# Kernel tuning notes

Hardware: AMD Instinct MI355X
Metric: run time of the kernel (lower is better)

## Reference

```python
import jax, jax.numpy as jnp
import numpy as np
from jax import lax

N_GAUSS = 32768
M_POINTS = 8192
BLOCK = 256
MAX_SCALE = 0.02
BG = -1.0


def setup_inputs() -> dict:
    key = jax.random.key(0)
    k = jax.random.split(key, 6)
    # query points in [-1, 1]^3 (forward maps them to [0,1]^3)
    x = jax.random.uniform(k[0], (M_POINTS, 3), jnp.float32) * 2.0 - 1.0
    xyz = jax.random.uniform(k[1], (N_GAUSS, 3), jnp.float32)          # means in [0,1]^3
    weight_raw = jax.random.normal(k[2], (N_GAUSS, 1), jnp.float32)
    scaling_raw = jax.random.normal(k[3], (N_GAUSS, 3), jnp.float32) * 0.3 + jnp.log(0.01)
    rotation_raw = jax.random.normal(k[4], (N_GAUSS, 4), jnp.float32)
    values_raw = jax.random.normal(k[5], (N_GAUSS, 1), jnp.float32)
    return {"x": x, "xyz": xyz, "weight_raw": weight_raw,
            "scaling_raw": scaling_raw, "rotation_raw": rotation_raw,
            "values_raw": values_raw}


def _quat_to_rotmat(q):
    # q: [N,4] normalized quaternion (w, x, y, z)
    w, x, y, z = q[:, 0], q[:, 1], q[:, 2], q[:, 3]
    r00 = 1 - 2 * (y * y + z * z); r01 = 2 * (x * y - w * z); r02 = 2 * (x * z + w * y)
    r10 = 2 * (x * y + w * z); r11 = 1 - 2 * (x * x + z * z); r12 = 2 * (y * z - w * x)
    r20 = 2 * (x * z - w * y); r21 = 2 * (y * z + w * x); r22 = 1 - 2 * (x * x + y * y)
    return jnp.stack([jnp.stack([r00, r01, r02], -1),
                      jnp.stack([r10, r11, r12], -1),
                      jnp.stack([r20, r21, r22], -1)], -2)  # [N,3,3]


def _splat(x, xyz, weight_raw, scaling_raw, rotation_raw, values_raw):
    p = (x + 1.0) / 2.0  # [M,3] in [0,1]^3
    # activations (match VEGS properties)
    s = jnp.exp(scaling_raw)                                  # [N,3]
    r = jnp.linalg.norm(s, axis=1, keepdims=True) + 1e-8
    r_soft = MAX_SCALE * jnp.tanh(r / MAX_SCALE)
    s = s * (r_soft / r)                                      # capped scales
    q = rotation_raw / (jnp.linalg.norm(rotation_raw, axis=1, keepdims=True) + 1e-12)
    R = _quat_to_rotmat(q)                                    # [N,3,3]
    inv_cov = jnp.einsum('nij,nj,nkj->nik', R, 1.0 / (s * s), R)  # Sigma^-1 = R S^-2 R^T
    w = jax.nn.sigmoid(weight_raw)[:, 0]                      # [N]
    v = jax.nn.sigmoid(values_raw)[:, 0]                      # [N]

    def block_fn(_, pb):
        # pb: [B,3]
        d = pb[:, None, :] - xyz[None, :, :]                  # [B,N,3]
        quad = jnp.einsum('bni,nij,bnj->bn', d, inv_cov, d)   # Mahalanobis^2
        alpha = w[None, :] * jnp.exp(-0.5 * quad)             # [B,N]
        num = alpha @ v                                       # [B]
        den = jnp.sum(alpha, axis=1)                          # [B]
        yb = jnp.where(den > 1e-8, num, BG)                   # empty cells -> bg = -1
        return None, yb

    nb = M_POINTS // BLOCK
    _, ys = lax.scan(block_fn, None, p.reshape(nb, BLOCK, 3))
    return ys.reshape(-1, 1)


def reference(x, xyz, weight_raw, scaling_raw, rotation_raw, values_raw):
    return _splat(x, xyz, weight_raw, scaling_raw, rotation_raw, values_raw)
```

## Files before the change

### kernel.cpp

```cpp
#include <hip/hip_runtime.h>

#define NG 32768
#define MP 8192
#define BG_VAL (-1.0f)
#define MAX_SCALE 0.02f

#define HALF_LOG2E 0.72134752044448170f
#define LOG2E      1.44269504088896340f

#define NC 4
#define NCELL (NC * NC * NC)
#define CELLW 0.25f
#define INV_CELLW 4.0f
#define RADF 7.899f

#define NSG 16
#define SCG 512
#define GCAP (NSG * SCG)
#define NSP 4
#define SCP 96
#define PCAP (NSP * SCP)

__device__ __forceinline__ float fast_rcp(float x)  { return __builtin_amdgcn_rcpf(x); }
__device__ __forceinline__ float fast_exp2(float x) { return __builtin_amdgcn_exp2f(x); }
__device__ __forceinline__ float fast_exp(float x)  { return fast_exp2(x * LOG2E); }
__device__ __forceinline__ float fast_sigmoid(float x) { return fast_rcp(1.0f + fast_exp(-x)); }

__global__ __launch_bounds__(256) void vegs_build(
    const float* __restrict__ x,
    const float* __restrict__ xyz,
    const float* __restrict__ weight_raw,
    const float* __restrict__ scaling_raw,
    const float* __restrict__ rotation_raw,
    const float* __restrict__ values_raw,
    float4* __restrict__ gp,
    float4* __restrict__ gr,
    float4* __restrict__ px4)
{
    const int tid = blockIdx.x * 256 + threadIdx.x;

    if (tid < NG) {
        const int n = tid;
        float s0 = fast_exp(scaling_raw[n * 3 + 0]);
        float s1 = fast_exp(scaling_raw[n * 3 + 1]);
        float s2 = fast_exp(scaling_raw[n * 3 + 2]);
        float r = sqrtf(s0 * s0 + s1 * s1 + s2 * s2) + 1e-8f;
        float y = r * (1.0f / MAX_SCALE);
        float E = fast_exp2(2.0f * LOG2E * y);
        float th = (E - 1.0f) * fast_rcp(E + 1.0f);
        float k = (MAX_SCALE * th) * fast_rcp(r);
        s0 *= k; s1 *= k; s2 *= k;

        float i0 = fast_rcp(s0 * s0);
        float i1 = fast_rcp(s1 * s1);
        float i2 = fast_rcp(s2 * s2);

        float qw = rotation_raw[n * 4 + 0];
        float qx = rotation_raw[n * 4 + 1];
        float qy = rotation_raw[n * 4 + 2];
        float qz = rotation_raw[n * 4 + 3];
        float qn = sqrtf(qw * qw + qx * qx + qy * qy + qz * qz) + 1e-12f;
        float iq = fast_rcp(qn);
        qw *= iq; qx *= iq; qy *= iq; qz *= iq;

        float r00 = 1.0f - 2.0f * (qy * qy + qz * qz);
        float r01 = 2.0f * (qx * qy - qw * qz);
        float r02 = 2.0f * (qx * qz + qw * qy);
        float r10 = 2.0f * (qx * qy + qw * qz);
        float r11 = 1.0f - 2.0f * (qx * qx + qz * qz);
        float r12 = 2.0f * (qy * qz - qw * qx);
        float r20 = 2.0f * (qx * qz - qw * qy);
        float r21 = 2.0f * (qy * qz + qw * qx);
        float r22 = 1.0f - 2.0f * (qx * qx + qy * qy);

        float G00 = r00 * r00 * i0 + r01 * r01 * i1 + r02 * r02 * i2;
        float G11 = r10 * r10 * i0 + r11 * r11 * i1 + r12 * r12 * i2;
        float G22 = r20 * r20 * i0 + r21 * r21 * i1 + r22 * r22 * i2;
        float G01 = r00 * r10 * i0 + r01 * r11 * i1 + r02 * r12 * i2;
        float G02 = r00 * r20 * i0 + r01 * r21 * i1 + r02 * r22 * i2;
        float G12 = r10 * r20 * i0 + r11 * r21 * i1 + r12 * r22 * i2;

        float w  = fast_sigmoid(weight_raw[n]);
        float v  = fast_sigmoid(values_raw[n]);
        float m0 = xyz[n * 3 + 0];
        float m1 = xyz[n * 3 + 1];
        float m2 = xyz[n * 3 + 2];

        const float c = HALF_LOG2E;
        float h0 = 2.0f * c * (G00 * m0 + G01 * m1 + G02 * m2);
        float h1 = 2.0f * c * (G01 * m0 + G11 * m1 + G12 * m2);
        float h2 = 2.0f * c * (G02 * m0 + G12 * m1 + G22 * m2);
        float k0 = -0.5f * (h0 * m0 + h1 * m1 + h2 * m2);

        gp[n * 3 + 0] = make_float4(-c * G00, -c * G11, -c * G22, -2.0f * c * G01);
        gp[n * 3 + 1] = make_float4(-2.0f * c * G02, -2.0f * c * G12, h0, h1);
        gp[n * 3 + 2] = make_float4(h2, k0, w, w * v);

        float smax = fmaxf(s0, fmaxf(s1, s2));
        gr[n] = make_float4(m0, m1, m2, RADF * smax);
    } else if (tid < NG + MP) {
        const int m = tid - NG;
        float p0 = (x[m * 3 + 0] + 1.0f) * 0.5f;
        float p1 = (x[m * 3 + 1] + 1.0f) * 0.5f;
        float p2 = (x[m * 3 + 2] + 1.0f) * 0.5f;
        int cx = min(NC - 1, max(0, (int)(p0 * INV_CELLW)));
        int cy = min(NC - 1, max(0, (int)(p1 * INV_CELLW)));
        int cz = min(NC - 1, max(0, (int)(p2 * INV_CELLW)));
        int cell = cx + NC * (cy + NC * cz);
        px4[m] = make_float4(p0, p1, p2, __int_as_float(cell));
    }
}

__global__ __launch_bounds__(64) void vegs_bin(
    const float4* __restrict__ gr,
    const float4* __restrict__ px4,
    unsigned short* __restrict__ glist,
    float4* __restrict__ spt,
    int* __restrict__ gcount,
    int* __restrict__ pcount)
{
    const int bid  = blockIdx.x;
    const int lane = threadIdx.x;

    if (bid < NCELL * NSG) {
        const int c = bid / NSG;
        const int s = bid - c * NSG;
        const int cx = c & 3, cy = (c >> 2) & 3, cz = c >> 4;
        const float lo0 = cx * CELLW, hi0 = lo0 + CELLW;
        const float lo1 = cy * CELLW, hi1 = lo1 + CELLW;
        const float lo2 = cz * CELLW, hi2 = lo2 + CELLW;
        unsigned short* __restrict__ slab = glist + (size_t)c * GCAP + s * SCG;

        const int beg = s * (NG / NSG);
        const int end = beg + (NG / NSG);
        int cnt = 0;
        #pragma unroll 4
        for (int base = beg; base < end; base += 64) {
            float4 g = gr[base + lane];
            float dx = fmaxf(fmaxf(lo0 - g.x, g.x - hi0), 0.0f);
            float dy = fmaxf(fmaxf(lo1 - g.y, g.y - hi1), 0.0f);
            float dz = fmaxf(fmaxf(lo2 - g.z, g.z - hi2), 0.0f);
            bool hit = (dx * dx + dy * dy + dz * dz) <= g.w * g.w;
            unsigned long long mask = __ballot(hit);
            int pos = cnt + __popcll(mask & ((1ULL << lane) - 1ULL));
            if (hit && pos < SCG) slab[pos] = (unsigned short)(base + lane);
            cnt += __popcll(mask);
        }
        if (lane == 0) gcount[c * NSG + s] = min(cnt, SCG);
    } else {
        const int pb = bid - NCELL * NSG;
        const int c = pb / NSP;
        const int s = pb - c * NSP;
        float4* __restrict__ slab = spt + (size_t)c * PCAP + s * SCP;

        const int beg = s * (MP / NSP);
        const int end = beg + (MP / NSP);
        int cnt = 0;
        #pragma unroll 4
        for (int base = beg; base < end; base += 64) {
            float4 P = px4[base + lane];
            bool hit = (__float_as_int(P.w) == c);
            unsigned long long mask = __ballot(hit);
            int pos = cnt + __popcll(mask & ((1ULL << lane) - 1ULL));
            if (hit && pos < SCP)
                slab[pos] = make_float4(P.x, P.y, P.z, __int_as_float(base + lane));
            cnt += __popcll(mask);
        }
        if (lane == 0) pcount[c * NSP + s] = min(cnt, SCP);
    }
}

__global__ __launch_bounds__(64) void vegs_cellmain(
    const float4* __restrict__ gp,
    const float4* __restrict__ spt,
    const unsigned short* __restrict__ glist,
    const int* __restrict__ gcount,
    const int* __restrict__ pcount,
    float2* __restrict__ partial)
{
    const int c    = blockIdx.x;
    const int yw   = blockIdx.y;
    const int k    = blockIdx.z;
    const int lane = threadIdx.x;
    const int s    = yw >> 1;
    const int half = yw & 1;

    const int np = pcount[c * NSP + s];
    if (half * 64 >= np) return;

    const int  pi     = half * 64 + lane;
    const bool active = pi < np;
    const int  slot   = c * PCAP + s * SCP + (active ? pi : np - 1);

    float4 P = spt[slot];
    const float p0 = P.x, p1 = P.y, p2 = P.z;

    const unsigned short* __restrict__ slab = glist + (size_t)c * GCAP + k * SCG;
    const int glen = gcount[c * NSG + k];

    float num = 0.0f, den = 0.0f;

    #pragma unroll 4
    for (int j = 0; j < glen; ++j) {
        int gid = slab[j];
        float4 A0 = gp[gid * 3 + 0];
        float4 A1 = gp[gid * 3 + 1];
        float4 A2 = gp[gid * 3 + 2];

        float t0 = fmaf(A0.x, p0, A1.z);
        t0 = fmaf(A0.w, p1, t0);
        t0 = fmaf(A1.x, p2, t0);
        float t1 = fmaf(A0.y, p1, A1.w);
        t1 = fmaf(A1.y, p2, t1);
        float t2 = fmaf(A0.z, p2, A2.x);
        float q = fmaf(p0, t0, A2.y);
        q = fmaf(p1, t1, q);
        q = fmaf(p2, t2, q);

        float e = fast_exp2(q);
        den = fmaf(A2.z, e, den);
        num = fmaf(A2.w, e, num);
    }

    if (active)
        partial[(size_t)k * (NCELL * PCAP) + c * PCAP + s * SCP + pi] =
            make_float2(num, den);
}

__global__ __launch_bounds__(256) void vegs_reduce(
    const float2* __restrict__ partial,
    const float4* __restrict__ spt,
    const int* __restrict__ pcount,
    float* __restrict__ out)
{
    const int slot = blockIdx.x * 256 + threadIdx.x;
    const int c   = slot / PCAP;
    const int rem = slot - c * PCAP;
    const int s   = rem / SCP;
    const int pi  = rem - s * SCP;
    if (pi >= pcount[c * NSP + s]) return;

    float num = 0.0f, den = 0.0f;
    #pragma unroll
    for (int k = 0; k < NSG; ++k) {
        float2 p = partial[(size_t)k * (NCELL * PCAP) + slot];
        num += p.x;
        den += p.y;
    }
    int orig = __float_as_int(spt[slot].w);
    out[orig] = (den > 1e-8f) ? num : BG_VAL;
}

extern "C" void kernel_launch(void* const* d_in, const int* in_sizes, int n_in,
                              void* d_out, int out_size, void* d_ws, size_t ws_size,
                              hipStream_t stream) {
    const float* x            = (const float*)d_in[0];
    const float* xyz          = (const float*)d_in[1];
    const float* weight_raw   = (const float*)d_in[2];
    const float* scaling_raw  = (const float*)d_in[3];
    const float* rotation_raw = (const float*)d_in[4];
    const float* values_raw   = (const float*)d_in[5];
    float* out = (float*)d_out;

    char* ws = (char*)d_ws;
    size_t off = 0;
    float4* gp    = (float4*)(ws + off); off += (size_t)NG * 3 * sizeof(float4);
    float4* gr    = (float4*)(ws + off); off += (size_t)NG * sizeof(float4);
    float4* px4   = (float4*)(ws + off); off += (size_t)MP * sizeof(float4);
    float4* spt   = (float4*)(ws + off); off += (size_t)NCELL * PCAP * sizeof(float4);
    float2* partial = (float2*)(ws + off); off += (size_t)NSG * NCELL * PCAP * sizeof(float2);
    unsigned short* glist = (unsigned short*)(ws + off); off += (size_t)NCELL * GCAP * 2;
    int* gcount = (int*)(ws + off); off += NCELL * NSG * sizeof(int);
    int* pcount = (int*)(ws + off); off += NCELL * NSP * sizeof(int);

    vegs_build<<<(NG + MP) / 256, 256, 0, stream>>>(
        x, xyz, weight_raw, scaling_raw, rotation_raw, values_raw, gp, gr, px4);

    vegs_bin<<<NCELL * NSG + NCELL * NSP, 64, 0, stream>>>(
        gr, px4, glist, spt, gcount, pcount);

    dim3 mg(NCELL, NSP * 2, NSG);
    vegs_cellmain<<<mg, 64, 0, stream>>>(gp, spt, glist, gcount, pcount, partial);

    vegs_reduce<<<NCELL * PCAP / 256, 256, 0, stream>>>(partial, spt, pcount, out);
}
```

Measured before the change: 119.1 us.

## Compact per-cell gaussian parameter slabs and process two points per thread

The binning pass now copies each hit gaussian's 48-byte parameter record into a contiguous per-cell slab, replacing the index list. The main loop therefore streams the slab sequentially instead of doing indirect gathers. Each thread evaluates two query points per gaussian load, using a compacted per-cell point index built from prefix sums of the sub-slab counts. The gaussian split changes from 16 slabs of 512 to 32 slabs of 256, and point cell classification moves from the build kernel into the bin kernel. This trades more workspace and bin-time writes for fewer loads per evaluation in the hot loop, and doubles the partial buffer the reduction reads.

```diff
diff --git a/kernel.cpp b/kernel.cpp
--- a/kernel.cpp
+++ b/kernel.cpp
@@ -9,13 +9,13 @@
 #define LOG2E      1.44269504088896340f
 
 #define NC 4
-#define NCELL (NC * NC * NC)
+#define NCELL 64
 #define CELLW 0.25f
 #define INV_CELLW 4.0f
 #define RADF 7.899f
 
-#define NSG 16
-#define SCG 512
+#define NSG 32
+#define SCG 256
 #define GCAP (NSG * SCG)
 #define NSP 4
 #define SCP 96
@@ -27,94 +27,81 @@
 __device__ __forceinline__ float fast_sigmoid(float x) { return fast_rcp(1.0f + fast_exp(-x)); }
 
 __global__ __launch_bounds__(256) void vegs_build(
-    const float* __restrict__ x,
     const float* __restrict__ xyz,
     const float* __restrict__ weight_raw,
     const float* __restrict__ scaling_raw,
     const float* __restrict__ rotation_raw,
     const float* __restrict__ values_raw,
     float4* __restrict__ gp,
-    float4* __restrict__ gr,
-    float4* __restrict__ px4)
+    float4* __restrict__ gr)
 {
-    const int tid = blockIdx.x * 256 + threadIdx.x;
-
-    if (tid < NG) {
-        const int n = tid;
-        float s0 = fast_exp(scaling_raw[n * 3 + 0]);
-        float s1 = fast_exp(scaling_raw[n * 3 + 1]);
-        float s2 = fast_exp(scaling_raw[n * 3 + 2]);
-        float r = sqrtf(s0 * s0 + s1 * s1 + s2 * s2) + 1e-8f;
-        float y = r * (1.0f / MAX_SCALE);
-        float E = fast_exp2(2.0f * LOG2E * y);
-        float th = (E - 1.0f) * fast_rcp(E + 1.0f);
-        float k = (MAX_SCALE * th) * fast_rcp(r);
-        s0 *= k; s1 *= k; s2 *= k;
-
-        float i0 = fast_rcp(s0 * s0);
-        float i1 = fast_rcp(s1 * s1);
-        float i2 = fast_rcp(s2 * s2);
-
-        float qw = rotation_raw[n * 4 + 0];
-        float qx = rotation_raw[n * 4 + 1];
-        float qy = rotation_raw[n * 4 + 2];
-        float qz = rotation_raw[n * 4 + 3];
-        float qn = sqrtf(qw * qw + qx * qx + qy * qy + qz * qz) + 1e-12f;
-        float iq = fast_rcp(qn);
-        qw *= iq; qx *= iq; qy *= iq; qz *= iq;
-
-        float r00 = 1.0f - 2.0f * (qy * qy + qz * qz);
-        float r01 = 2.0f * (qx * qy - qw * qz);
-        float r02 = 2.0f * (qx * qz + qw * qy);
-        float r10 = 2.0f * (qx * qy + qw * qz);
-        float r11 = 1.0f - 2.0f * (qx * qx + qz * qz);
-        float r12 = 2.0f * (qy * qz - qw * qx);
-        float r20 = 2.0f * (qx * qz - qw * qy);
-        float r21 = 2.0f * (qy * qz + qw * qx);
-        float r22 = 1.0f - 2.0f * (qx * qx + qy * qy);
-
-        float G00 = r00 * r00 * i0 + r01 * r01 * i1 + r02 * r02 * i2;
-        float G11 = r10 * r10 * i0 + r11 * r11 * i1 + r12 * r12 * i2;
-        float G22 = r20 * r20 * i0 + r21 * r21 * i1 + r22 * r22 * i2;
-        float G01 = r00 * r10 * i0 + r01 * r11 * i1 + r02 * r12 * i2;
-        float G02 = r00 * r20 * i0 + r01 * r21 * i1 + r02 * r22 * i2;
-        float G12 = r10 * r20 * i0 + r11 * r21 * i1 + r12 * r22 * i2;
-
-        float w  = fast_sigmoid(weight_raw[n]);
-        float v  = fast_sigmoid(values_raw[n]);
-        float m0 = xyz[n * 3 + 0];
-        float m1 = xyz[n * 3 + 1];
-        float m2 = xyz[n * 3 + 2];
-
-        const float c = HALF_LOG2E;
-        float h0 = 2.0f * c * (G00 * m0 + G01 * m1 + G02 * m2);
-        float h1 = 2.0f * c * (G01 * m0 + G11 * m1 + G12 * m2);
-        float h2 = 2.0f * c * (G02 * m0 + G12 * m1 + G22 * m2);
-        float k0 = -0.5f * (h0 * m0 + h1 * m1 + h2 * m2);
-
-        gp[n * 3 + 0] = make_float4(-c * G00, -c * G11, -c * G22, -2.0f * c * G01);
-        gp[n * 3 + 1] = make_float4(-2.0f * c * G02, -2.0f * c * G12, h0, h1);
-        gp[n * 3 + 2] = make_float4(h2, k0, w, w * v);
-
-        float smax = fmaxf(s0, fmaxf(s1, s2));
-        gr[n] = make_float4(m0, m1, m2, RADF * smax);
-    } else if (tid < NG + MP) {
-        const int m = tid - NG;
-        float p0 = (x[m * 3 + 0] + 1.0f) * 0.5f;
-        float p1 = (x[m * 3 + 1] + 1.0f) * 0.5f;
-        float p2 = (x[m * 3 + 2] + 1.0f) * 0.5f;
-        int cx = min(NC - 1, max(0, (int)(p0 * INV_CELLW)));
-        int cy = min(NC - 1, max(0, (int)(p1 * INV_CELLW)));
-        int cz = min(NC - 1, max(0, (int)(p2 * INV_CELLW)));
-        int cell = cx + NC * (cy + NC * cz);
-        px4[m] = make_float4(p0, p1, p2, __int_as_float(cell));
-    }
+    const int n = blockIdx.x * 256 + threadIdx.x;
+    if (n >= NG) return;
+
+    float s0 = fast_exp(scaling_raw[n * 3 + 0]);
+    float s1 = fast_exp(scaling_raw[n * 3 + 1]);
+    float s2 = fast_exp(scaling_raw[n * 3 + 2]);
+    float r = sqrtf(s0 * s0 + s1 * s1 + s2 * s2) + 1e-8f;
+    float y = r * (1.0f / MAX_SCALE);
+    float E = fast_exp2(2.0f * LOG2E * y);
+    float th = (E - 1.0f) * fast_rcp(E + 1.0f);
+    float k = (MAX_SCALE * th) * fast_rcp(r);
+    s0 *= k; s1 *= k; s2 *= k;
+
+    float i0 = fast_rcp(s0 * s0);
+    float i1 = fast_rcp(s1 * s1);
+    float i2 = fast_rcp(s2 * s2);
+
+    float qw = rotation_raw[n * 4 + 0];
+    float qx = rotation_raw[n * 4 + 1];
+    float qy = rotation_raw[n * 4 + 2];
+    float qz = rotation_raw[n * 4 + 3];
+    float qn = sqrtf(qw * qw + qx * qx + qy * qy + qz * qz) + 1e-12f;
+    float iq = fast_rcp(qn);
+    qw *= iq; qx *= iq; qy *= iq; qz *= iq;
+
+    float r00 = 1.0f - 2.0f * (qy * qy + qz * qz);
+    float r01 = 2.0f * (qx * qy - qw * qz);
+    float r02 = 2.0f * (qx * qz + qw * qy);
+    float r10 = 2.0f * (qx * qy + qw * qz);
+    float r11 = 1.0f - 2.0f * (qx * qx + qz * qz);
+    float r12 = 2.0f * (qy * qz - qw * qx);
+    float r20 = 2.0f * (qx * qz - qw * qy);
+    float r21 = 2.0f * (qy * qz + qw * qx);
+    float r22 = 1.0f - 2.0f * (qx * qx + qy * qy);
+
+    float G00 = r00 * r00 * i0 + r01 * r01 * i1 + r02 * r02 * i2;
+    float G11 = r10 * r10 * i0 + r11 * r11 * i1 + r12 * r12 * i2;
+    float G22 = r20 * r20 * i0 + r21 * r21 * i1 + r22 * r22 * i2;
+    float G01 = r00 * r10 * i0 + r01 * r11 * i1 + r02 * r12 * i2;
+    float G02 = r00 * r20 * i0 + r01 * r21 * i1 + r02 * r22 * i2;
+    float G12 = r10 * r20 * i0 + r11 * r21 * i1 + r12 * r22 * i2;
+
+    float w  = fast_sigmoid(weight_raw[n]);
+    float v  = fast_sigmoid(values_raw[n]);
+    float m0 = xyz[n * 3 + 0];
+    float m1 = xyz[n * 3 + 1];
+    float m2 = xyz[n * 3 + 2];
+
+    const float c = HALF_LOG2E;
+    float h0 = 2.0f * c * (G00 * m0 + G01 * m1 + G02 * m2);
+    float h1 = 2.0f * c * (G01 * m0 + G11 * m1 + G12 * m2);
+    float h2 = 2.0f * c * (G02 * m0 + G12 * m1 + G22 * m2);
+    float k0 = -0.5f * (h0 * m0 + h1 * m1 + h2 * m2);
+
+    gp[n * 3 + 0] = make_float4(-c * G00, -c * G11, -c * G22, -2.0f * c * G01);
+    gp[n * 3 + 1] = make_float4(-2.0f * c * G02, -2.0f * c * G12, h0, h1);
+    gp[n * 3 + 2] = make_float4(h2, k0, w, w * v);
+
+    float smax = fmaxf(s0, fmaxf(s1, s2));
+    gr[n] = make_float4(m0, m1, m2, RADF * smax);
 }
 
 __global__ __launch_bounds__(64) void vegs_bin(
+    const float* __restrict__ x,
     const float4* __restrict__ gr,
-    const float4* __restrict__ px4,
-    unsigned short* __restrict__ glist,
+    const float4* __restrict__ gp,
+    float4* __restrict__ cslab,
     float4* __restrict__ spt,
     int* __restrict__ gcount,
     int* __restrict__ pcount)
@@ -129,24 +116,29 @@
         const float lo0 = cx * CELLW, hi0 = lo0 + CELLW;
         const float lo1 = cy * CELLW, hi1 = lo1 + CELLW;
         const float lo2 = cz * CELLW, hi2 = lo2 + CELLW;
-        unsigned short* __restrict__ slab = glist + (size_t)c * GCAP + s * SCG;
+        float4* __restrict__ slab = cslab + ((size_t)c * GCAP + s * SCG) * 3;
 
         const int beg = s * (NG / NSG);
         const int end = beg + (NG / NSG);
         int cnt = 0;
         #pragma unroll 4
         for (int base = beg; base < end; base += 64) {
-            float4 g = gr[base + lane];
+            const int gid = base + lane;
+            float4 g = gr[gid];
             float dx = fmaxf(fmaxf(lo0 - g.x, g.x - hi0), 0.0f);
             float dy = fmaxf(fmaxf(lo1 - g.y, g.y - hi1), 0.0f);
             float dz = fmaxf(fmaxf(lo2 - g.z, g.z - hi2), 0.0f);
             bool hit = (dx * dx + dy * dy + dz * dz) <= g.w * g.w;
             unsigned long long mask = __ballot(hit);
             int pos = cnt + __popcll(mask & ((1ULL << lane) - 1ULL));
-            if (hit && pos < SCG) slab[pos] = (unsigned short)(base + lane);
+            if (hit && pos < SCG) {
+                slab[pos * 3 + 0] = gp[gid * 3 + 0];
+                slab[pos * 3 + 1] = gp[gid * 3 + 1];
+                slab[pos * 3 + 2] = gp[gid * 3 + 2];
+            }
             cnt += __popcll(mask);
         }
-        if (lane == 0) gcount[c * NSG + s] = min(cnt, SCG);
+        if (lane == 0) gcount[bid] = min(cnt, SCG);
     } else {
         const int pb = bid - NCELL * NSG;
         const int c = pb / NSP;
@@ -158,73 +150,102 @@
         int cnt = 0;
         #pragma unroll 4
         for (int base = beg; base < end; base += 64) {
-            float4 P = px4[base + lane];
-            bool hit = (__float_as_int(P.w) == c);
+            const int m = base + lane;
+            float p0 = (x[m * 3 + 0] + 1.0f) * 0.5f;
+            float p1 = (x[m * 3 + 1] + 1.0f) * 0.5f;
+            float p2 = (x[m * 3 + 2] + 1.0f) * 0.5f;
+            int cx = min(NC - 1, max(0, (int)(p0 * INV_CELLW)));
+            int cy = min(NC - 1, max(0, (int)(p1 * INV_CELLW)));
+            int cz = min(NC - 1, max(0, (int)(p2 * INV_CELLW)));
+            bool hit = (cx + NC * (cy + NC * cz)) == c;
             unsigned long long mask = __ballot(hit);
             int pos = cnt + __popcll(mask & ((1ULL << lane) - 1ULL));
             if (hit && pos < SCP)
-                slab[pos] = make_float4(P.x, P.y, P.z, __int_as_float(base + lane));
+                slab[pos] = make_float4(p0, p1, p2, __int_as_float(m));
             cnt += __popcll(mask);
         }
-        if (lane == 0) pcount[c * NSP + s] = min(cnt, SCP);
+        if (lane == 0) pcount[pb] = min(cnt, SCP);
     }
 }
 
 __global__ __launch_bounds__(64) void vegs_cellmain(
-    const float4* __restrict__ gp,
+    const float4* __restrict__ cslab,
     const float4* __restrict__ spt,
-    const unsigned short* __restrict__ glist,
     const int* __restrict__ gcount,
     const int* __restrict__ pcount,
     float2* __restrict__ partial)
 {
     const int c    = blockIdx.x;
-    const int yw   = blockIdx.y;
+    const int pb   = blockIdx.y;
     const int k    = blockIdx.z;
     const int lane = threadIdx.x;
-    const int s    = yw >> 1;
-    const int half = yw & 1;
-
-    const int np = pcount[c * NSP + s];
-    if (half * 64 >= np) return;
-
-    const int  pi     = half * 64 + lane;
-    const bool active = pi < np;
-    const int  slot   = c * PCAP + s * SCP + (active ? pi : np - 1);
-
-    float4 P = spt[slot];
-    const float p0 = P.x, p1 = P.y, p2 = P.z;
-
-    const unsigned short* __restrict__ slab = glist + (size_t)c * GCAP + k * SCG;
+
+    const int n0 = pcount[c * NSP + 0];
+    const int n1 = pcount[c * NSP + 1];
+    const int n2 = pcount[c * NSP + 2];
+    const int n3 = pcount[c * NSP + 3];
+    const int c1 = n0, c2 = c1 + n1, c3 = c2 + n2;
+    const int nt = c3 + n3;
+    if (pb * 128 >= nt) return;
+
+    const int  piA  = pb * 128 + lane;
+    const int  piB  = piA + 64;
+    const bool actA = piA < nt;
+    const bool actB = piB < nt;
+    const int  peA  = actA ? piA : 0;
+    const int  peB  = actB ? piB : 0;
+
+    int sA = (peA >= c1) + (peA >= c2) + (peA >= c3);
+    int cumA = (sA == 0) ? 0 : ((sA == 1) ? c1 : ((sA == 2) ? c2 : c3));
+    int sB = (peB >= c1) + (peB >= c2) + (peB >= c3);
+    int cumB = (sB == 0) ? 0 : ((sB == 1) ? c1 : ((sB == 2) ? c2 : c3));
+
+    float4 PA = spt[c * PCAP + sA * SCP + (peA - cumA)];
+    float4 PB = spt[c * PCAP + sB * SCP + (peB - cumB)];
+    const float a0 = PA.x, a1 = PA.y, a2 = PA.z;
+    const float b0 = PB.x, b1 = PB.y, b2 = PB.z;
+
+    const float4* __restrict__ base = cslab + ((size_t)c * GCAP + k * SCG) * 3;
     const int glen = gcount[c * NSG + k];
 
-    float num = 0.0f, den = 0.0f;
+    float numA = 0.0f, denA = 0.0f;
+    float numB = 0.0f, denB = 0.0f;
 
     #pragma unroll 4
     for (int j = 0; j < glen; ++j) {
-        int gid = slab[j];
-        float4 A0 = gp[gid * 3 + 0];
-        float4 A1 = gp[gid * 3 + 1];
-        float4 A2 = gp[gid * 3 + 2];
-
-        float t0 = fmaf(A0.x, p0, A1.z);
-        t0 = fmaf(A0.w, p1, t0);
-        t0 = fmaf(A1.x, p2, t0);
-        float t1 = fmaf(A0.y, p1, A1.w);
-        t1 = fmaf(A1.y, p2, t1);
-        float t2 = fmaf(A0.z, p2, A2.x);
-        float q = fmaf(p0, t0, A2.y);
-        q = fmaf(p1, t1, q);
-        q = fmaf(p2, t2, q);
-
-        float e = fast_exp2(q);
-        den = fmaf(A2.z, e, den);
-        num = fmaf(A2.w, e, num);
+        float4 A0 = base[j * 3 + 0];
+        float4 A1 = base[j * 3 + 1];
+        float4 A2 = base[j * 3 + 2];
+
+        float t0 = fmaf(A0.x, a0, A1.z);
+        t0 = fmaf(A0.w, a1, t0);
+        t0 = fmaf(A1.x, a2, t0);
+        float t1 = fmaf(A0.y, a1, A1.w);
+        t1 = fmaf(A1.y, a2, t1);
+        float t2 = fmaf(A0.z, a2, A2.x);
+        float qA = fmaf(a0, t0, A2.y);
+        qA = fmaf(a1, t1, qA);
+        qA = fmaf(a2, t2, qA);
+        float eA = fast_exp2(qA);
+        denA = fmaf(A2.z, eA, denA);
+        numA = fmaf(A2.w, eA, numA);
+
+        float u0 = fmaf(A0.x, b0, A1.z);
+        u0 = fmaf(A0.w, b1, u0);
+        u0 = fmaf(A1.x, b2, u0);
+        float u1 = fmaf(A0.y, b1, A1.w);
+        u1 = fmaf(A1.y, b2, u1);
+        float u2 = fmaf(A0.z, b2, A2.x);
+        float qB = fmaf(b0, u0, A2.y);
+        qB = fmaf(b1, u1, qB);
+        qB = fmaf(b2, u2, qB);
+        float eB = fast_exp2(qB);
+        denB = fmaf(A2.z, eB, denB);
+        numB = fmaf(A2.w, eB, numB);
     }
 
-    if (active)
-        partial[(size_t)k * (NCELL * PCAP) + c * PCAP + s * SCP + pi] =
-            make_float2(num, den);
+    if (actA) partial[(size_t)k * (NCELL * PCAP) + c * PCAP + piA] = make_float2(numA, denA);
+    if (actB) partial[(size_t)k * (NCELL * PCAP) + c * PCAP + piB] = make_float2(numB, denB);
 }
 
 __global__ __launch_bounds__(256) void vegs_reduce(
@@ -233,21 +254,29 @@
     const int* __restrict__ pcount,
     float* __restrict__ out)
 {
-    const int slot = blockIdx.x * 256 + threadIdx.x;
-    const int c   = slot / PCAP;
-    const int rem = slot - c * PCAP;
-    const int s   = rem / SCP;
-    const int pi  = rem - s * SCP;
-    if (pi >= pcount[c * NSP + s]) return;
+    const int g  = blockIdx.x * 256 + threadIdx.x;
+    const int c  = g / PCAP;
+    const int pi = g - c * PCAP;
+
+    const int n0 = pcount[c * NSP + 0];
+    const int n1 = pcount[c * NSP + 1];
+    const int n2 = pcount[c * NSP + 2];
+    const int n3 = pcount[c * NSP + 3];
+    const int c1 = n0, c2 = c1 + n1, c3 = c2 + n2;
+    const int nt = c3 + n3;
+    if (pi >= nt) return;
 
     float num = 0.0f, den = 0.0f;
-    #pragma unroll
+    #pragma unroll 8
     for (int k = 0; k < NSG; ++k) {
-        float2 p = partial[(size_t)k * (NCELL * PCAP) + slot];
+        float2 p = partial[(size_t)k * (NCELL * PCAP) + g];
         num += p.x;
         den += p.y;
     }
-    int orig = __float_as_int(spt[slot].w);
+
+    int s = (pi >= c1) + (pi >= c2) + (pi >= c3);
+    int cum = (s == 0) ? 0 : ((s == 1) ? c1 : ((s == 2) ? c2 : c3));
+    int orig = __float_as_int(spt[c * PCAP + s * SCP + (pi - cum)].w);
     out[orig] = (den > 1e-8f) ? num : BG_VAL;
 }
 
@@ -266,21 +295,20 @@
     size_t off = 0;
     float4* gp    = (float4*)(ws + off); off += (size_t)NG * 3 * sizeof(float4);
     float4* gr    = (float4*)(ws + off); off += (size_t)NG * sizeof(float4);
-    float4* px4   = (float4*)(ws + off); off += (size_t)MP * sizeof(float4);
     float4* spt   = (float4*)(ws + off); off += (size_t)NCELL * PCAP * sizeof(float4);
+    float4* cslab = (float4*)(ws + off); off += (size_t)NCELL * GCAP * 3 * sizeof(float4);
     float2* partial = (float2*)(ws + off); off += (size_t)NSG * NCELL * PCAP * sizeof(float2);
-    unsigned short* glist = (unsigned short*)(ws + off); off += (size_t)NCELL * GCAP * 2;
-    int* gcount = (int*)(ws + off); off += NCELL * NSG * sizeof(int);
-    int* pcount = (int*)(ws + off); off += NCELL * NSP * sizeof(int);
-
-    vegs_build<<<(NG + MP) / 256, 256, 0, stream>>>(
-        x, xyz, weight_raw, scaling_raw, rotation_raw, values_raw, gp, gr, px4);
+    int* gcount = (int*)(ws + off); off += (size_t)NCELL * NSG * sizeof(int);
+    int* pcount = (int*)(ws + off); off += (size_t)NCELL * NSP * sizeof(int);
+
+    vegs_build<<<NG / 256, 256, 0, stream>>>(
+        xyz, weight_raw, scaling_raw, rotation_raw, values_raw, gp, gr);
 
     vegs_bin<<<NCELL * NSG + NCELL * NSP, 64, 0, stream>>>(
-        gr, px4, glist, spt, gcount, pcount);
-
-    dim3 mg(NCELL, NSP * 2, NSG);
-    vegs_cellmain<<<mg, 64, 0, stream>>>(gp, spt, glist, gcount, pcount, partial);
+        x, gr, gp, cslab, spt, gcount, pcount);
+
+    dim3 mg(NCELL, PCAP / 128, NSG);
+    vegs_cellmain<<<mg, 64, 0, stream>>>(cslab, spt, gcount, pcount, partial);
 
     vegs_reduce<<<NCELL * PCAP / 256, 256, 0, stream>>>(partial, spt, pcount, out);
 }
```

New measurement: 104.1 us. 1.14x faster.
